# Kernel tuning notes

Hardware: AMD Instinct MI355X
Metric: run time of the kernel (lower is better)

## Reference

```python
import jax, jax.numpy as jnp
from jax import lax
import numpy as np

C, CK, CV, K = 256, 32, 32, 3  # channels, key_channels, value_channels, kernel_size
B, H, W = 8, 128, 128


def setup_inputs() -> dict:
    key = jax.random.key(0)
    ks = jax.random.split(key, 12)
    s = 0.05
    return {
        "x": jax.random.normal(ks[0], (B, C, H, W), jnp.float32),
        # key branch: 1x1 conv C->CK (+ReLU), depthwise 3x3 CK->CK, 1x1 conv CK->K*K
        "k1_w": jax.random.normal(ks[1], (CK, C), jnp.float32) * s,
        "k1_b": jax.random.normal(ks[2], (CK,), jnp.float32) * s,
        "dw_w": jax.random.normal(ks[3], (CK, 1, K, K), jnp.float32) * s,
        "dw_b": jax.random.normal(ks[4], (CK,), jnp.float32) * s,
        "k3_w": jax.random.normal(ks[5], (K * K, CK), jnp.float32) * s,
        "k3_b": jax.random.normal(ks[6], (K * K,), jnp.float32) * s,
        # value branch: 1x1 conv C->CV (no act)
        "v_w": jax.random.normal(ks[7], (CV, C), jnp.float32) * s,
        "v_b": jax.random.normal(ks[8], (CV,), jnp.float32) * s,
        # out conv: 1x1 CV->C (no act)
        "o_w": jax.random.normal(ks[9], (C, CV), jnp.float32) * s,
        "o_b": jax.random.normal(ks[10], (C,), jnp.float32) * s,
    }


def _conv1x1(t, w, b):
    # t: [B,Cin,H,W], w: [Cout,Cin] -> [B,Cout,H,W]
    return jnp.einsum("bchw,oc->bohw", t, w) + b[None, :, None, None]


def reference(x, k1_w, k1_b, dw_w, dw_b, k3_w, k3_b, v_w, v_b, o_w, o_b):
    b, _, h, w = x.shape
    pad = (K - 1) // 2
    # ---- key branch ----
    k = jax.nn.relu(_conv1x1(x, k1_w, k1_b))
    k = lax.conv_general_dilated(
        k, dw_w, window_strides=(1, 1), padding=[(pad, pad), (pad, pad)],
        dimension_numbers=("NCHW", "OIHW", "NCHW"), feature_group_count=CK,
    ) + dw_b[None, :, None, None]
    k = _conv1x1(k, k3_w, k3_b)                      # [B, K*K, H, W]
    weights = jax.nn.softmax(k, axis=1)[:, None]     # [B, 1, K*K, H, W]
    # ---- value branch: 1x1 conv then unfold (3x3 neighborhoods, pad 1) ----
    v = _conv1x1(x, v_w, v_b)                        # [B, CV, H, W]
    vp = jnp.pad(v, ((0, 0), (0, 0), (pad, pad), (pad, pad)))
    # torch Unfold ordering: per-channel, kernel offsets row-major
    patches = jnp.stack(
        [vp[:, :, i : i + h, j : j + w] for i in range(K) for j in range(K)],
        axis=2,
    )                                                # [B, CV, K*K, H, W]
    y = jnp.sum(weights * patches, axis=2)           # [B, CV, H, W]
    y = _conv1x1(y, o_w, o_b)                        # [B, C, H, W]
    return x + y
```

## Files before the change

### kernel.cpp

```cpp
#include <hip/hip_runtime.h>
#include <cmath>

namespace {
constexpr int Cc = 256, CKc = 32, CVc = 32, KKc = 9;
constexpr int Bc = 8, Hc = 128, Wc = 128, HWc = Hc * Wc;

typedef __attribute__((ext_vector_type(8))) short   s16x8;
typedef __attribute__((ext_vector_type(8))) __bf16  bf16x8;
typedef __attribute__((ext_vector_type(4))) float   f32x4;

__device__ inline unsigned short f2bf(float f) {
    union { float f; unsigned u; } v; v.f = f;
    unsigned u = v.u + 0x7fffu + ((v.u >> 16) & 1u);
    return (unsigned short)(u >> 16);
}
}

__global__ __launch_bounds__(256) void ns_k1v(
    const float* __restrict__ x,
    const float* __restrict__ k1_w, const float* __restrict__ k1_b,
    const float* __restrict__ v_w,  const float* __restrict__ v_b,
    const float* __restrict__ o_w,
    unsigned short* __restrict__ k1pm, unsigned short* __restrict__ vpm,
    unsigned short* __restrict__ owbf)
{
    constexpr int LP = 72;
    __shared__ short w_bf[64][LP];
    __shared__ short x_bf[128][LP];

    const int tid = threadIdx.x;
    const int l   = tid & 63;
    const int li  = l & 15;
    const int lk  = l >> 4;
    const int wv  = __builtin_amdgcn_readfirstlane(tid >> 6);

    if (blockIdx.x == 0) {
        for (int i = tid * 4; i < Cc * CVc; i += 256 * 4) {
            const float4 f = *(const float4*)(o_w + i);
            const unsigned a = (unsigned)f2bf(f.x) | ((unsigned)f2bf(f.y) << 16);
            const unsigned c = (unsigned)f2bf(f.z) | ((unsigned)f2bf(f.w) << 16);
            *(uint2*)(owbf + i) = make_uint2(a, c);
        }
    }

    const int flat0 = blockIdx.x * 128;
    const int b  = flat0 / HWc;
    const int pp = flat0 - b * HWc;
    const float* xb = x + (size_t)b * Cc * HWc + pp;

    const int spx  = tid & 127;
    const int schh = tid >> 7;
    const int so   = tid & 63;
    const int swc0 = (tid >> 6) * 16;
    const float* wsrc = (so < 32) ? (k1_w + (size_t)so * Cc)
                                  : (v_w + (size_t)(so - 32) * Cc);

    f32x4 acc[8];
    const f32x4 zero = {0.f, 0.f, 0.f, 0.f};
#pragma unroll
    for (int i = 0; i < 8; ++i) acc[i] = zero;

    for (int c0 = 0; c0 < Cc; c0 += 64) {
        __syncthreads();
        {
            alignas(16) short tmp[16];
#pragma unroll
            for (int f = 0; f < 4; ++f) {
                const float4 fv = *(const float4*)(wsrc + c0 + swc0 + f * 4);
                tmp[f*4+0] = f2bf(fv.x); tmp[f*4+1] = f2bf(fv.y);
                tmp[f*4+2] = f2bf(fv.z); tmp[f*4+3] = f2bf(fv.w);
            }
            *(s16x8*)&w_bf[so][swc0]     = *(const s16x8*)&tmp[0];
            *(s16x8*)&w_bf[so][swc0 + 8] = *(const s16x8*)&tmp[8];
        }
#pragma unroll
        for (int u = 0; u < 8; ++u) {
            const int ch = (schh * 8 + u) * 4;
            const float e0 = xb[(size_t)(c0 + ch + 0) * HWc + spx];
            const float e1 = xb[(size_t)(c0 + ch + 1) * HWc + spx];
            const float e2 = xb[(size_t)(c0 + ch + 2) * HWc + spx];
            const float e3 = xb[(size_t)(c0 + ch + 3) * HWc + spx];
            const unsigned p01 = (unsigned)f2bf(e0) | ((unsigned)f2bf(e1) << 16);
            const unsigned p23 = (unsigned)f2bf(e2) | ((unsigned)f2bf(e3) << 16);
            *(uint2*)&x_bf[spx][ch] = make_uint2(p01, p23);
        }
        __syncthreads();

#pragma unroll
        for (int ks = 0; ks < 2; ++ks) {
            const s16x8 ar = *(const s16x8*)&w_bf[wv * 16 + li][ks * 32 + lk * 8];
            const bf16x8 af = __builtin_bit_cast(bf16x8, ar);
#pragma unroll
            for (int pt = 0; pt < 8; ++pt) {
                const s16x8 br = *(const s16x8*)&x_bf[pt * 16 + li][ks * 32 + lk * 8];
                acc[pt] = __builtin_amdgcn_mfma_f32_16x16x32_bf16(
                    af, __builtin_bit_cast(bf16x8, br), acc[pt], 0, 0, 0);
            }
        }
    }

    const bool is_k = wv < 2;
    const int obase = wv * 16 + lk * 4;
    const int chq = is_k ? obase : obase - 32;
    float bias[4];
#pragma unroll
    for (int r = 0; r < 4; ++r)
        bias[r] = is_k ? k1_b[obase + r] : v_b[obase + r - 32];
    unsigned short* dstb = is_k ? k1pm : vpm;

#pragma unroll
    for (int pt = 0; pt < 8; ++pt) {
        const size_t row = (size_t)b * HWc + pp + pt * 16 + li;
        float v0 = acc[pt][0] + bias[0], v1 = acc[pt][1] + bias[1];
        float v2 = acc[pt][2] + bias[2], v3 = acc[pt][3] + bias[3];
        if (is_k) {
            v0 = fmaxf(v0, 0.f); v1 = fmaxf(v1, 0.f);
            v2 = fmaxf(v2, 0.f); v3 = fmaxf(v3, 0.f);
        }
        const unsigned p01 = (unsigned)f2bf(v0) | ((unsigned)f2bf(v1) << 16);
        const unsigned p23 = (unsigned)f2bf(v2) | ((unsigned)f2bf(v3) << 16);
        *(uint2*)(dstb + row * 32 + chq) = make_uint2(p01, p23);
    }
}

__global__ __launch_bounds__(512, 4) void ns_fused(
    const float* __restrict__ x,
    const unsigned short* __restrict__ k1pm,
    const unsigned short* __restrict__ vpm,
    const float* __restrict__ dw_w, const float* __restrict__ dw_b,
    const float* __restrict__ k3_w, const float* __restrict__ k3_b,
    const unsigned short* __restrict__ owbf, const float* __restrict__ o_b,
    float* __restrict__ out)
{
    constexpr int PX = 256;
    constexpr int WPAD = 40;
    __shared__ short y_lds[PX][WPAD];
    __shared__ float plds[2][KKc][PX];
    __shared__ float dwt[KKc][CKc];
    __shared__ float k3s[KKc][CKc];
    __shared__ float dwbs[CKc];
    __shared__ float k3bs[KKc];

    const int tid = threadIdx.x;
    if (tid < CKc * KKc) {
        const int ck = tid / KKc, kk = tid - ck * KKc;
        dwt[kk][ck] = dw_w[tid];
        ((float*)k3s)[tid] = k3_w[tid];
    }
    if (tid < CKc) dwbs[tid] = dw_b[tid];
    if (tid < KKc) k3bs[tid] = k3_b[tid];
    __syncthreads();

    const int pxi  = tid & 255;
    const int half = tid >> 8;
    const int cb   = half * 16;

    const int flat0 = blockIdx.x * PX;
    const int b  = flat0 / HWc;
    const int p0 = flat0 - b * HWc;
    const int p  = p0 + pxi;
    const int h  = p / Wc;
    const int w  = p - h * Wc;

    const unsigned short* k1b = k1pm + (size_t)b * HWc * 32;
    const unsigned short* vb  = vpm  + (size_t)b * HWc * 32;

    float t[16];
#pragma unroll
    for (int e = 0; e < 16; ++e) t[e] = dwbs[cb + e];
#pragma unroll
    for (int i = 0; i < 3; ++i) {
        const int hh = h + i - 1;
#pragma unroll
        for (int j = 0; j < 3; ++j) {
            const int ww = w + j - 1;
            if (hh < 0 || hh >= Hc || ww < 0 || ww >= Wc) continue;
            const unsigned short* kr = k1b + (size_t)(hh * Wc + ww) * 32 + cb;
            const int ij = i * 3 + j;
#pragma unroll
            for (int qv = 0; qv < 2; ++qv) {
                const bf16x8 kv = __builtin_bit_cast(bf16x8, *(const s16x8*)(kr + qv * 8));
#pragma unroll
                for (int e = 0; e < 8; ++e)
                    t[qv * 8 + e] = fmaf((float)kv[e], dwt[ij][cb + qv * 8 + e],
                                         t[qv * 8 + e]);
            }
        }
    }

#pragma unroll
    for (int kk = 0; kk < KKc; ++kk) {
        float a = (half == 0) ? k3bs[kk] : 0.f;
#pragma unroll
        for (int e = 0; e < 16; ++e)
            a = fmaf(k3s[kk][cb + e], t[e], a);
        plds[half][kk][pxi] = a;
    }
    __syncthreads();

    float logit[KKc];
#pragma unroll
    for (int kk = 0; kk < KKc; ++kk)
        logit[kk] = plds[0][kk][pxi] + plds[1][kk][pxi];

    float m = logit[0];
#pragma unroll
    for (int kk = 1; kk < KKc; ++kk) m = fmaxf(m, logit[kk]);
    float s = 0.f;
#pragma unroll
    for (int kk = 0; kk < KKc; ++kk) { logit[kk] = expf(logit[kk] - m); s += logit[kk]; }
    const float inv = 1.f / s;
#pragma unroll
    for (int kk = 0; kk < KKc; ++kk) logit[kk] *= inv;

    float yv[16];
#pragma unroll
    for (int e = 0; e < 16; ++e) yv[e] = 0.f;
#pragma unroll
    for (int i = 0; i < 3; ++i) {
        const int hh = h + i - 1;
#pragma unroll
        for (int j = 0; j < 3; ++j) {
            const int ww = w + j - 1;
            if (hh < 0 || hh >= Hc || ww < 0 || ww >= Wc) continue;
            const unsigned short* vr = vb + (size_t)(hh * Wc + ww) * 32 + cb;
            const float wv = logit[i * 3 + j];
#pragma unroll
            for (int qv = 0; qv < 2; ++qv) {
                const bf16x8 vv = __builtin_bit_cast(bf16x8, *(const s16x8*)(vr + qv * 8));
#pragma unroll
                for (int e = 0; e < 8; ++e)
                    yv[qv * 8 + e] = fmaf(wv, (float)vv[e], yv[qv * 8 + e]);
            }
        }
    }

    {
        alignas(16) short ybf[16];
#pragma unroll
        for (int e = 0; e < 16; ++e) ybf[e] = (short)f2bf(yv[e]);
        *(float4*)&y_lds[pxi][cb]     = *(const float4*)&ybf[0];
        *(float4*)&y_lds[pxi][cb + 8] = *(const float4*)&ybf[8];
    }
    __syncthreads();

    const int wvv = tid >> 6;
    const int l  = tid & 63;
    const int li = l & 15;
    const int lk = l >> 4;

    const float* xb0 = x + (size_t)b * Cc * HWc;
    float* ob0 = out + (size_t)b * Cc * HWc;

#pragma unroll
    for (int i = 0; i < 2; ++i) {
        const int ot = wvv * 2 + i;
        const int och = ot * 16 + li;
        const s16x8 wr8 = *(const s16x8*)(owbf + (size_t)och * 32 + lk * 8);
        const bf16x8 wfrag = __builtin_bit_cast(bf16x8, wr8);
        const float bias = o_b[och];
        const float* xrow = xb0 + (size_t)och * HWc;
        float* orow = ob0 + (size_t)och * HWc;
#pragma unroll
        for (int pt = 0; pt < 16; ++pt) {
            const s16x8 yr8 = *(const s16x8*)&y_lds[pt * 16 + li][lk * 8];
            const bf16x8 yfrag = __builtin_bit_cast(bf16x8, yr8);
            f32x4 acc = {0.f, 0.f, 0.f, 0.f};
            acc = __builtin_amdgcn_mfma_f32_16x16x32_bf16(yfrag, wfrag, acc, 0, 0, 0);
            const int px0 = p0 + pt * 16 + lk * 4;
            const float4 xv = *(const float4*)(xrow + px0);
            float4 ov;
            ov.x = xv.x + acc[0] + bias;
            ov.y = xv.y + acc[1] + bias;
            ov.z = xv.z + acc[2] + bias;
            ov.w = xv.w + acc[3] + bias;
            *(float4*)(orow + px0) = ov;
        }
    }
}

extern "C" void kernel_launch(void* const* d_in, const int* in_sizes, int n_in,
                              void* d_out, int out_size, void* d_ws, size_t ws_size,
                              hipStream_t stream)
{
    const float* x    = (const float*)d_in[0];
    const float* k1_w = (const float*)d_in[1];
    const float* k1_b = (const float*)d_in[2];
    const float* dw_w = (const float*)d_in[3];
    const float* dw_b = (const float*)d_in[4];
    const float* k3_w = (const float*)d_in[5];
    const float* k3_b = (const float*)d_in[6];
    const float* v_w  = (const float*)d_in[7];
    const float* v_b  = (const float*)d_in[8];
    const float* o_w  = (const float*)d_in[9];
    const float* o_b  = (const float*)d_in[10];
    float* out = (float*)d_out;

    unsigned short* k1pm = (unsigned short*)d_ws;
    unsigned short* vpm  = k1pm + (size_t)Bc * HWc * 32;
    unsigned short* owbf = vpm  + (size_t)Bc * HWc * 32;

    const int npx = Bc * HWc;

    ns_k1v <<<dim3(npx / 128), dim3(256), 0, stream>>>(x, k1_w, k1_b, v_w, v_b, o_w,
                                                       k1pm, vpm, owbf);
    ns_fused<<<dim3(npx / 256), dim3(512), 0, stream>>>(x, k1pm, vpm, dw_w, dw_b,
                                                        k3_w, k3_b, owbf, o_b, out);
}
```

Baseline: 100.1 us.

## Split fused attention kernel into y-computation and output-conv kernels with swizzled rows

Splits the fused kernel into two. The first computes the softmax-weighted neighbourhood sum y per image row and writes it to a bf16 workspace, with a block-index swizzle that interleaves batches. The second runs the 1x1 output conv via MFMA plus the residual add, with each wave reusing a y fragment across four output tiles. The aim is to cut LDS use and raise occupancy in each stage, at the cost of an extra launch and a global write and read of y.

```diff
diff --git a/kernel.cpp b/kernel.cpp
--- a/kernel.cpp
+++ b/kernel.cpp
@@ -123,19 +123,14 @@
     }
 }
 
-__global__ __launch_bounds__(512, 4) void ns_fused(
-    const float* __restrict__ x,
+__global__ __launch_bounds__(256) void ns_y(
     const unsigned short* __restrict__ k1pm,
     const unsigned short* __restrict__ vpm,
     const float* __restrict__ dw_w, const float* __restrict__ dw_b,
     const float* __restrict__ k3_w, const float* __restrict__ k3_b,
-    const unsigned short* __restrict__ owbf, const float* __restrict__ o_b,
-    float* __restrict__ out)
+    unsigned short* __restrict__ ypm)
 {
-    constexpr int PX = 256;
-    constexpr int WPAD = 40;
-    __shared__ short y_lds[PX][WPAD];
-    __shared__ float plds[2][KKc][PX];
+    __shared__ float plds[2][KKc][128];
     __shared__ float dwt[KKc][CKc];
     __shared__ float k3s[KKc][CKc];
     __shared__ float dwbs[CKc];
@@ -147,20 +142,28 @@
         dwt[kk][ck] = dw_w[tid];
         ((float*)k3s)[tid] = k3_w[tid];
     }
+    for (int idx = 256 + tid; idx < CKc * KKc; idx += 256) {
+        const int ck = idx / KKc, kk = idx - ck * KKc;
+        dwt[kk][ck] = dw_w[idx];
+        ((float*)k3s)[idx] = k3_w[idx];
+    }
     if (tid < CKc) dwbs[tid] = dw_b[tid];
     if (tid < KKc) k3bs[tid] = k3_b[tid];
     __syncthreads();
 
-    const int pxi  = tid & 255;
-    const int half = tid >> 8;
+    const int bid = blockIdx.x;
+    const int swz = (bid & 7) * 128 + (bid >> 3);
+
+    const int pxi  = tid & 127;
+    const int half = tid >> 7;
     const int cb   = half * 16;
 
-    const int flat0 = blockIdx.x * PX;
-    const int b  = flat0 / HWc;
-    const int p0 = flat0 - b * HWc;
-    const int p  = p0 + pxi;
-    const int h  = p / Wc;
-    const int w  = p - h * Wc;
+    const int flat0 = swz * 128;
+    const int b   = flat0 / HWc;
+    const int row = flat0 - b * HWc;
+    const int h   = row >> 7;
+    const int w   = pxi;
+    const int p   = row + pxi;
 
     const unsigned short* k1b = k1pm + (size_t)b * HWc * 32;
     const unsigned short* vb  = vpm  + (size_t)b * HWc * 32;
@@ -235,46 +238,64 @@
         }
     }
 
-    {
-        alignas(16) short ybf[16];
-#pragma unroll
-        for (int e = 0; e < 16; ++e) ybf[e] = (short)f2bf(yv[e]);
-        *(float4*)&y_lds[pxi][cb]     = *(const float4*)&ybf[0];
-        *(float4*)&y_lds[pxi][cb + 8] = *(const float4*)&ybf[8];
-    }
-    __syncthreads();
-
+    alignas(16) short ybf[16];
+#pragma unroll
+    for (int e = 0; e < 16; ++e) ybf[e] = (short)f2bf(yv[e]);
+    unsigned short* yo = ypm + ((size_t)b * HWc + p) * 32 + cb;
+    *(float4*)(yo)     = *(const float4*)&ybf[0];
+    *(float4*)(yo + 8) = *(const float4*)&ybf[8];
+}
+
+__global__ __launch_bounds__(256) void ns_oconv(
+    const float* __restrict__ x,
+    const unsigned short* __restrict__ ypm,
+    const unsigned short* __restrict__ owbf, const float* __restrict__ o_b,
+    float* __restrict__ out)
+{
+    const int tid = threadIdx.x;
     const int wvv = tid >> 6;
     const int l  = tid & 63;
     const int li = l & 15;
     const int lk = l >> 4;
 
+    const int flat0 = blockIdx.x * 128;
+    const int b  = flat0 / HWc;
+    const int p0 = flat0 - b * HWc;
+
+    const unsigned short* yb = ypm + ((size_t)b * HWc + p0) * 32;
     const float* xb0 = x + (size_t)b * Cc * HWc;
     float* ob0 = out + (size_t)b * Cc * HWc;
 
-#pragma unroll
-    for (int i = 0; i < 2; ++i) {
-        const int ot = wvv * 2 + i;
-        const int och = ot * 16 + li;
-        const s16x8 wr8 = *(const s16x8*)(owbf + (size_t)och * 32 + lk * 8);
-        const bf16x8 wfrag = __builtin_bit_cast(bf16x8, wr8);
-        const float bias = o_b[och];
-        const float* xrow = xb0 + (size_t)och * HWc;
-        float* orow = ob0 + (size_t)och * HWc;
-#pragma unroll
-        for (int pt = 0; pt < 16; ++pt) {
-            const s16x8 yr8 = *(const s16x8*)&y_lds[pt * 16 + li][lk * 8];
-            const bf16x8 yfrag = __builtin_bit_cast(bf16x8, yr8);
+    bf16x8 wfrag[4];
+    float  bias[4];
+    const float* xrow[4];
+    float* orow[4];
+#pragma unroll
+    for (int i = 0; i < 4; ++i) {
+        const int och = (wvv * 4 + i) * 16 + li;
+        wfrag[i] = __builtin_bit_cast(bf16x8,
+                     *(const s16x8*)(owbf + (size_t)och * 32 + lk * 8));
+        bias[i] = o_b[och];
+        xrow[i] = xb0 + (size_t)och * HWc;
+        orow[i] = ob0 + (size_t)och * HWc;
+    }
+
+#pragma unroll
+    for (int pt = 0; pt < 8; ++pt) {
+        const bf16x8 yfrag = __builtin_bit_cast(bf16x8,
+            *(const s16x8*)(yb + (size_t)(pt * 16 + li) * 32 + lk * 8));
+        const int px0 = p0 + pt * 16 + lk * 4;
+#pragma unroll
+        for (int i = 0; i < 4; ++i) {
             f32x4 acc = {0.f, 0.f, 0.f, 0.f};
-            acc = __builtin_amdgcn_mfma_f32_16x16x32_bf16(yfrag, wfrag, acc, 0, 0, 0);
-            const int px0 = p0 + pt * 16 + lk * 4;
-            const float4 xv = *(const float4*)(xrow + px0);
+            acc = __builtin_amdgcn_mfma_f32_16x16x32_bf16(yfrag, wfrag[i], acc, 0, 0, 0);
+            const float4 xv = *(const float4*)(xrow[i] + px0);
             float4 ov;
-            ov.x = xv.x + acc[0] + bias;
-            ov.y = xv.y + acc[1] + bias;
-            ov.z = xv.z + acc[2] + bias;
-            ov.w = xv.w + acc[3] + bias;
-            *(float4*)(orow + px0) = ov;
+            ov.x = xv.x + acc[0] + bias[i];
+            ov.y = xv.y + acc[1] + bias[i];
+            ov.z = xv.z + acc[2] + bias[i];
+            ov.w = xv.w + acc[3] + bias[i];
+            *(float4*)(orow[i] + px0) = ov;
         }
     }
 }
@@ -298,12 +319,14 @@
 
     unsigned short* k1pm = (unsigned short*)d_ws;
     unsigned short* vpm  = k1pm + (size_t)Bc * HWc * 32;
-    unsigned short* owbf = vpm  + (size_t)Bc * HWc * 32;
+    unsigned short* ypm  = vpm  + (size_t)Bc * HWc * 32;
+    unsigned short* owbf = ypm  + (size_t)Bc * HWc * 32;
 
     const int npx = Bc * HWc;
 
-    ns_k1v <<<dim3(npx / 128), dim3(256), 0, stream>>>(x, k1_w, k1_b, v_w, v_b, o_w,
-                                                       k1pm, vpm, owbf);
-    ns_fused<<<dim3(npx / 256), dim3(512), 0, stream>>>(x, k1pm, vpm, dw_w, dw_b,
-                                                        k3_w, k3_b, owbf, o_b, out);
-}
+    ns_k1v  <<<dim3(npx / 128), dim3(256), 0, stream>>>(x, k1_w, k1_b, v_w, v_b, o_w,
+                                                        k1pm, vpm, owbf);
+    ns_y    <<<dim3(npx / 128), dim3(256), 0, stream>>>(k1pm, vpm, dw_w, dw_b,
+                                                        k3_w, k3_b, ypm);
+    ns_oconv<<<dim3(npx / 128), dim3(256), 0, stream>>>(x, ypm, owbf, o_b, out);
+}
```

Result: slower. 116.6 us (+16.5%).
